# Kernel optimization log

Hardware: AMD Instinct MI355X
Metric: run time of the kernel (lower is better)

Reference implementation:

```python
import jax, jax.numpy as jnp
import numpy as np


def _pairwise_upper_dists(x):
    # x: [N, D] -> distances for all i<j pairs, shape [N*(N-1)/2]
    n = x.shape[0]
    sq = jnp.sum(x * x, axis=-1)                      # [N]
    d2 = sq[:, None] + sq[None, :] - 2.0 * (x @ x.T)  # [N, N]
    d2 = jnp.maximum(d2, 0.0)
    iu, ju = jnp.triu_indices(n, k=1)                 # matches combinations(range(n), 2)
    return jnp.sqrt(d2[iu, ju])


def setup_inputs() -> dict:
    key = jax.random.key(0)
    k1, k2 = jax.random.split(key)
    pred = jax.random.normal(k1, (1024, 8192), dtype=jnp.float32)
    target = jax.random.normal(k2, (1024, 8192), dtype=jnp.float32)
    return {"pred": pred, "target": target}


def reference(pred, target):
    # all_pairs_in_batch=True branch: Euclidean distance per pair, MSE between
    # the pred-distance vector and the target-distance vector.
    pred_d = _pairwise_upper_dists(pred)      # [P]
    target_d = _pairwise_upper_dists(target)  # [P]
    return jnp.mean((pred_d - target_d) ** 2)
```

## Files before the change

### kernel.cpp

```cpp
#include <hip/hip_runtime.h>
#include <hip/hip_bf16.h>
#include <hip/hip_fp16.h>

#define D 8192
#define NPAIR 523776.0

typedef short short8 __attribute__((ext_vector_type(8)));
typedef float f32x4 __attribute__((ext_vector_type(4)));
typedef _Float16 f16x8 __attribute__((ext_vector_type(8)));
typedef int int32x4 __attribute__((ext_vector_type(4)));

#define GLOAD_LDS(G, L) __builtin_amdgcn_global_load_lds( \
    (const __attribute__((address_space(1))) void*)(G),   \
    (__attribute__((address_space(3))) void*)(L), 16, 0, 0)

__device__ __forceinline__ short8 cvt8(const float4 a, const float4 b) {
    union { short8 s; __hip_bfloat162 h[4]; } u;
    u.h[0] = __float22bfloat162_rn(make_float2(a.x, a.y));
    u.h[1] = __float22bfloat162_rn(make_float2(a.z, a.w));
    u.h[2] = __float22bfloat162_rn(make_float2(b.x, b.y));
    u.h[3] = __float22bfloat162_rn(make_float2(b.z, b.w));
    return u.s;
}

__device__ __forceinline__ int q8(float x) {
    return __float2int_rn(fminf(fmaxf(x * 32.f, -127.f), 127.f));
}
__device__ __forceinline__ int pack4(float a, float b, float c, float d) {
    return (q8(a) & 255) | ((q8(b) & 255) << 8) | ((q8(c) & 255) << 16) | ((q8(d) & 255) << 24);
}

__device__ __forceinline__ void decode_bid(int bid, int& m, int& ti, int& tj, int& k0, int& nsteps) {
    int x = bid & 7, s = bid >> 3;
    m = x >> 2;
    int xr = x & 3;
    if (s < 16) {
        ti = tj = s & 7;
        int c = ((s >> 3) << 2) + xr;
        k0 = c * 1024; nsteps = 16;
    } else {
        int sp = s - 16;
        int c = (sp / 28) * 4 + xr;
        int tt = sp % 28;
        int a = 0;
        while (tt >= 7 - a) { tt -= 7 - a; ++a; }
        ti = a; tj = a + 1 + tt;
        k0 = c * 512; nsteps = 8;
    }
}
__device__ __forceinline__ int bid_off(int m, int tt, int c) {
    return (m * 4 + (c & 3)) + ((16 + (c >> 2) * 28 + tt) << 3);
}
__device__ __forceinline__ int bid_diag(int m, int dt, int c) {
    return (m * 4 + (c & 3)) + ((((c >> 2) << 3) + dt) << 3);
}

__global__ __launch_bounds__(256)
void convert_kernel(const float* __restrict__ pred, const float* __restrict__ tgt,
                    char* __restrict__ q) {
    const int idx = blockIdx.x * 256 + threadIdx.x;
    const int t = idx & 511;
    const int c = idx >> 9;
    const int m = c >> 10, p = (c >> 7) & 7, ks = c & 127;
    const int rl = t >> 2;
    const int s = (t & 3) ^ ((rl >> 1) & 3);
    const float* __restrict__ src = (m ? tgt : pred) + (size_t)(p * 128 + rl) * D + ks * 64 + s * 16;
    const float4 a = ((const float4*)src)[0];
    const float4 b = ((const float4*)src)[1];
    const float4 e = ((const float4*)src)[2];
    const float4 f = ((const float4*)src)[3];
    int32x4 o;
    o[0] = pack4(a.x, a.y, a.z, a.w);
    o[1] = pack4(b.x, b.y, b.z, b.w);
    o[2] = pack4(e.x, e.y, e.z, e.w);
    o[3] = pack4(f.x, f.y, f.z, f.w);
    *(int32x4*)(q + (size_t)c * 8192 + t * 16) = o;
}

#define STAGE(S, COFF) { \
    GLOAD_LDS(gAc + (size_t)(S) * 8192 + gsub, lsb + (COFF) + wid * 1024); \
    if (!same) GLOAD_LDS(gBc + (size_t)(S) * 8192 + gsub, lsb + (COFF) + 8192 + wid * 1024); \
}

#define GSTEP { \
    if (sp + 1 < nsteps) STAGE(sp + 1, cN); \
    { \
        const char* __restrict__ bA = lsb + cC; \
        const char* __restrict__ bB = lsb + cC + boff; \
        __builtin_amdgcn_s_setprio(1); \
        int32x4 b0 = *(const int32x4*)(bB + rbB + kby); \
        int32x4 b1 = *(const int32x4*)(bB + rbB + 1024 + kby); \
        _Pragma("unroll") \
        for (int mi = 0; mi < 4; ++mi) { \
            int32x4 af = *(const int32x4*)(bA + rbA + mi * 1024 + kby); \
            acc[mi][0] = __builtin_amdgcn_mfma_i32_16x16x64_i8(af, b0, acc[mi][0], 0, 0, 0); \
            acc[mi][1] = __builtin_amdgcn_mfma_i32_16x16x64_i8(af, b1, acc[mi][1], 0, 0, 0); \
        } \
        __builtin_amdgcn_s_setprio(0); \
    } \
    asm volatile("s_waitcnt vmcnt(0)" ::: "memory"); \
    __builtin_amdgcn_s_barrier(); \
    { int t_ = cC; cC = cN; cN = t_; } \
    ++sp; \
}

__global__ __launch_bounds__(512, 4)
void gram_kernel(const char* __restrict__ q, __half* __restrict__ part,
                 float* __restrict__ norms) {
    int m, ti, tj, k0, nsteps;
    decode_bid(blockIdx.x, m, ti, tj, k0, nsteps);
    const bool same = (ti == tj);

    __shared__ short ls[16384];
    char* lsb = (char*)ls;

    const int tid = threadIdx.x;
    const int lane = tid & 63;
    const int wid = tid >> 6;
    const int wr = wid >> 2, wc = wid & 3;

    const char* __restrict__ gAc = q + (size_t)(m * 1024 + ti * 128 + (k0 >> 6)) * 8192;
    const char* __restrict__ gBc = q + (size_t)(m * 1024 + tj * 128 + (k0 >> 6)) * 8192;
    const int gsub = wid * 1024 + lane * 16;

    const int boff = same ? 0 : 8192;
    const int rbA = (wr * 64 + (lane & 15)) * 64;
    const int rbB = (wc * 32 + (lane & 15)) * 64;
    const int kby = (((lane >> 4) ^ (((lane & 15) >> 1) & 3)) << 4);

    int32x4 zero = {0, 0, 0, 0};
    int32x4 acc[4][2];
#pragma unroll
    for (int mi = 0; mi < 4; ++mi) { acc[mi][0] = zero; acc[mi][1] = zero; }

    int cC = 0, cN = 16384;

    STAGE(0, cC)
    asm volatile("s_waitcnt vmcnt(0)" ::: "memory");
    __builtin_amdgcn_s_barrier();

    int sp = 0;
    while (sp < nsteps) { GSTEP }

    __half* __restrict__ dst = part + (size_t)blockIdx.x * 16384;
#pragma unroll
    for (int mi = 0; mi < 4; ++mi)
#pragma unroll
        for (int ni = 0; ni < 2; ++ni)
#pragma unroll
            for (int r = 0; r < 4; ++r) {
                int li = wr * 64 + mi * 16 + (lane >> 4) * 4 + r;
                int lj = wc * 32 + ni * 16 + (lane & 15);
                float g = (float)acc[mi][ni][r] * (1.f / 1024.f);
                dst[li * 128 + lj] = __float2half_rn(g);
                if (same && li == lj)
                    atomicAdd(&norms[m * 1024 + ti * 128 + li], g);
            }
}

__global__ __launch_bounds__(256)
void loss_store_kernel(const __half* __restrict__ part, const float* __restrict__ norms,
                       float* __restrict__ partial) {
    const int tid = threadIdx.x;
    const int sid = blockIdx.x * 256 + tid;
    const int i  = sid >> 7;
    const int j0 = (sid & 127) << 3;
    float local = 0.f;
    if (j0 + 7 > i) {
        const int ti = i >> 7, tj = j0 >> 7;
        const int el = ((i & 127) << 7) + (j0 & 127);
        float gp[8] = {0,0,0,0,0,0,0,0}, gt[8] = {0,0,0,0,0,0,0,0};
        if (ti == tj) {
#pragma unroll
            for (int c = 0; c < 8; ++c) {
                f16x8 vp = *(const f16x8*)(part + (size_t)bid_diag(0, ti, c) * 16384 + el);
                f16x8 vt = *(const f16x8*)(part + (size_t)bid_diag(1, ti, c) * 16384 + el);
#pragma unroll
                for (int e = 0; e < 8; ++e) { gp[e] += (float)vp[e]; gt[e] += (float)vt[e]; }
            }
        } else {
            int tt = 7 * ti - (ti * (ti - 1)) / 2 + (tj - ti - 1);
#pragma unroll
            for (int c = 0; c < 16; ++c) {
                f16x8 vp = *(const f16x8*)(part + (size_t)bid_off(0, tt, c) * 16384 + el);
                f16x8 vt = *(const f16x8*)(part + (size_t)bid_off(1, tt, c) * 16384 + el);
#pragma unroll
                for (int e = 0; e < 8; ++e) { gp[e] += (float)vp[e]; gt[e] += (float)vt[e]; }
            }
        }
        const float nip = norms[i], nit = norms[1024 + i];
        const float4 njp0 = *(const float4*)(norms + j0);
        const float4 njp1 = *(const float4*)(norms + j0 + 4);
        const float4 njt0 = *(const float4*)(norms + 1024 + j0);
        const float4 njt1 = *(const float4*)(norms + 1024 + j0 + 4);
        const float njp[8] = {njp0.x, njp0.y, njp0.z, njp0.w, njp1.x, njp1.y, njp1.z, njp1.w};
        const float njt[8] = {njt0.x, njt0.y, njt0.z, njt0.w, njt1.x, njt1.y, njt1.z, njt1.w};
#pragma unroll
        for (int e = 0; e < 8; ++e) {
            int j = j0 + e;
            if (j > i) {
                float dp = nip + njp[e] - 2.f * gp[e];
                float dt = nit + njt[e] - 2.f * gt[e];
                float c2 = sqrtf(fmaxf(dp, 0.f)) - sqrtf(fmaxf(dt, 0.f));
                local += c2 * c2;
            }
        }
    }
#pragma unroll
    for (int off = 32; off > 0; off >>= 1) local += __shfl_down(local, off);
    __shared__ float wsum[4];
    if ((tid & 63) == 0) wsum[tid >> 6] = local;
    __syncthreads();
    if (tid == 0) partial[blockIdx.x] = wsum[0] + wsum[1] + wsum[2] + wsum[3];
}

template<int NPART>
__global__ __launch_bounds__(256)
void finalize_kernel(const float* __restrict__ partial, float* __restrict__ out) {
    const int tid = threadIdx.x;
    double local = 0.0;
#pragma unroll
    for (int k = 0; k < NPART / 256; ++k) local += (double)partial[tid + k * 256];
#pragma unroll
    for (int off = 32; off > 0; off >>= 1) local += __shfl_down(local, off);
    __shared__ double wsum[4];
    if ((tid & 63) == 0) wsum[tid >> 6] = local;
    __syncthreads();
    if (tid == 0) out[0] = (float)((wsum[0] + wsum[1] + wsum[2] + wsum[3]) / NPAIR);
}

__device__ __forceinline__ void decode_bid_fb(int bid, int& m, int& ti, int& tj, int& k0, int& nsteps) {
    int x = bid & 7, s = bid >> 3;
    m = x >> 2;
    int xr = x & 3;
    if (s < 16) {
        ti = tj = s & 7;
        int c = ((s >> 3) << 2) + xr;
        k0 = c * 1024; nsteps = 32;
    } else {
        int sp = s - 16;
        int c = (sp / 28) * 4 + xr;
        int tt = sp % 28;
        int a = 0;
        while (tt >= 7 - a) { tt -= 7 - a; ++a; }
        ti = a; tj = a + 1 + tt;
        k0 = c * 512; nsteps = 16;
    }
}

__global__ __launch_bounds__(512)
void gram_fb(const float* __restrict__ pred, const float* __restrict__ tgt,
             float* __restrict__ g4) {
    int m, ti, tj, k0, nsteps;
    decode_bid_fb(blockIdx.x, m, ti, tj, k0, nsteps);
    const bool same = (ti == tj);
    const float* __restrict__ x = m ? tgt : pred;
    __shared__ short lsA[2][4096];
    __shared__ short lsB[2][4096];
    const int tid = threadIdx.x;
    const int lane = tid & 63;
    const int wid = tid >> 6;
    const int wr = wid >> 2, wc = wid & 3;
    const int srow = tid >> 2, sc8 = tid & 3;
    const float* __restrict__ gA = x + (size_t)(ti * 128 + srow) * D + k0 + sc8 * 8;
    const float* __restrict__ gB = x + (size_t)(tj * 128 + srow) * D + k0 + sc8 * 8;
    const int wby = srow * 64 + ((sc8 ^ ((srow >> 1) & 3)) << 4);
    const int rbA = (wr * 64 + (lane & 15)) * 64;
    const int rbB = (wc * 32 + (lane & 15)) * 64;
    const int kby = (((lane >> 4) ^ (((lane & 15) >> 1) & 3)) << 4);
    f32x4 zero = {0.f, 0.f, 0.f, 0.f};
    f32x4 acc[4][2];
#pragma unroll
    for (int mi = 0; mi < 4; ++mi) { acc[mi][0] = zero; acc[mi][1] = zero; }
    float4 ra0, ra1, rb0, rb1;
    { const float4* p = (const float4*)gA; ra0 = p[0]; ra1 = p[1];
      if (!same) { const float4* qq = (const float4*)gB; rb0 = qq[0]; rb1 = qq[1]; } }
    *(short8*)((char*)lsA[0] + wby) = cvt8(ra0, ra1);
    if (!same) *(short8*)((char*)lsB[0] + wby) = cvt8(rb0, rb1);
    { const float4* p = (const float4*)(gA + 32); ra0 = p[0]; ra1 = p[1];
      if (!same) { const float4* qq = (const float4*)(gB + 32); rb0 = qq[0]; rb1 = qq[1]; } }
    asm volatile("s_waitcnt lgkmcnt(0)" ::: "memory");
    __builtin_amdgcn_s_barrier();
    for (int step = 0; step < nsteps; ++step) {
        const int cur = step & 1;
        const short* __restrict__ bufA = lsA[cur];
        const short* __restrict__ bufB = same ? lsA[cur] : lsB[cur];
        short8 bf0 = *(const short8*)((const char*)bufB + (rbB + kby));
        short8 bf1 = *(const short8*)((const char*)bufB + (rbB + 1024 + kby));
#pragma unroll
        for (int mi = 0; mi < 4; ++mi) {
            short8 af = *(const short8*)((const char*)bufA + (rbA + mi * 1024 + kby));
            acc[mi][0] = __builtin_amdgcn_mfma_f32_16x16x32_bf16(af, bf0, acc[mi][0], 0, 0, 0);
            acc[mi][1] = __builtin_amdgcn_mfma_f32_16x16x32_bf16(af, bf1, acc[mi][1], 0, 0, 0);
        }
        if (step + 1 < nsteps) {
            const int nxt = cur ^ 1;
            *(short8*)((char*)lsA[nxt] + wby) = cvt8(ra0, ra1);
            if (!same) *(short8*)((char*)lsB[nxt] + wby) = cvt8(rb0, rb1);
            if (step + 2 < nsteps) {
                const float4* p = (const float4*)(gA + (step + 2) * 32);
                ra0 = p[0]; ra1 = p[1];
                if (!same) { const float4* qq = (const float4*)(gB + (step + 2) * 32); rb0 = qq[0]; rb1 = qq[1]; }
            }
        }
        asm volatile("s_waitcnt lgkmcnt(0)" ::: "memory");
        __builtin_amdgcn_s_barrier();
    }
#pragma unroll
    for (int mi = 0; mi < 4; ++mi)
#pragma unroll
        for (int ni = 0; ni < 2; ++ni)
#pragma unroll
            for (int r = 0; r < 4; ++r) {
                int gi = ti * 128 + wr * 64 + mi * 16 + (lane >> 4) * 4 + r;
                int gj = tj * 128 + wc * 32 + ni * 16 + (lane & 15);
                atomicAdd(&g4[(size_t)m * 1048576 + gi * 1024 + gj], acc[mi][ni][r]);
            }
}

__global__ __launch_bounds__(256)
void loss_atomic_kernel(const float* __restrict__ gram, float* __restrict__ partial) {
    const float* __restrict__ gP = gram;
    const float* __restrict__ gT = gram + 1024 * 1024;
    const int tid = threadIdx.x;
    const int base = blockIdx.x * 256 + tid;
    float local = 0.f;
#pragma unroll
    for (int s = 0; s < 4; ++s) {
        int lin = base + s * 262144;
        int i = lin >> 10, j = lin & 1023;
        if (j > i) {
            float dp = gP[i * 1024 + i] + gP[j * 1024 + j] - 2.f * gP[lin];
            float dt = gT[i * 1024 + i] + gT[j * 1024 + j] - 2.f * gT[lin];
            float c = sqrtf(fmaxf(dp, 0.f)) - sqrtf(fmaxf(dt, 0.f));
            local += c * c;
        }
    }
#pragma unroll
    for (int off = 32; off > 0; off >>= 1) local += __shfl_down(local, off);
    __shared__ float wsum[4];
    if ((tid & 63) == 0) wsum[tid >> 6] = local;
    __syncthreads();
    if (tid == 0) partial[blockIdx.x] = wsum[0] + wsum[1] + wsum[2] + wsum[3];
}

extern "C" void kernel_launch(void* const* d_in, const int* in_sizes, int n_in,
                              void* d_out, int out_size, void* d_ws, size_t ws_size,
                              hipStream_t stream) {
    const float* pred = (const float*)d_in[0];
    const float* tgt  = (const float*)d_in[1];
    const size_t q_bytes    = (size_t)2048 * 8192;
    const size_t part_bytes = (size_t)1024 * 16384 * 2;
    const size_t need = q_bytes + part_bytes + (2048 + 512) * sizeof(float);
    if (ws_size >= need) {
        char* qbuf     = (char*)d_ws;
        __half* part   = (__half*)((char*)d_ws + q_bytes);
        float* norms   = (float*)((char*)part + part_bytes);
        float* partial = norms + 2048;
        hipMemsetAsync(norms, 0, 2048 * sizeof(float), stream);
        convert_kernel<<<4096, 256, 0, stream>>>(pred, tgt, qbuf);
        gram_kernel<<<1024, 512, 0, stream>>>(qbuf, part, norms);
        loss_store_kernel<<<512, 256, 0, stream>>>(part, norms, partial);
        finalize_kernel<512><<<1, 256, 0, stream>>>(partial, (float*)d_out);
    } else {
        float* gram    = (float*)d_ws;
        float* partial = (float*)d_ws + (size_t)2 * 1024 * 1024;
        hipMemsetAsync(gram, 0, (size_t)2 * 1024 * 1024 * sizeof(float), stream);
        gram_fb<<<1024, 512, 0, stream>>>(pred, tgt, gram);
        loss_atomic_kernel<<<1024, 256, 0, stream>>>(gram, partial);
        finalize_kernel<1024><<<1, 256, 0, stream>>>(partial, (float*)d_out);
    }
}
```

Measured before the change: 48.50 us.

## Split gram K-range across twice as many blocks with single-shot LDS load

Doubles the number of gram blocks by halving each block's K slab (diagonal blocks cover 8 slabs, off-diagonal 4). Each block now loads its whole slab into a larger 64KB LDS buffer at once and computes without a double-buffered pipeline. This spreads work over more CUs and cuts the per-block serial steps. In exchange the loss kernel must reduce twice as many fp16 partial tiles, and the partial buffer doubles in size. The larger LDS footprint may also lower occupancy.

```diff
diff --git a/kernel.cpp b/kernel.cpp
--- a/kernel.cpp
+++ b/kernel.cpp
@@ -30,26 +30,26 @@
     return (q8(a) & 255) | ((q8(b) & 255) << 8) | ((q8(c) & 255) << 16) | ((q8(d) & 255) << 24);
 }
 
-__device__ __forceinline__ void decode_bid(int bid, int& m, int& ti, int& tj, int& k0, int& nsteps) {
+__device__ __forceinline__ void decode_bid(int bid, int& m, int& ti, int& tj, int& ks0, bool& diag) {
     int x = bid & 7, s = bid >> 3;
     m = x >> 2;
     int xr = x & 3;
-    if (s < 16) {
+    if (s < 32) {
         ti = tj = s & 7;
         int c = ((s >> 3) << 2) + xr;
-        k0 = c * 1024; nsteps = 16;
-    } else {
-        int sp = s - 16;
-        int c = (sp / 28) * 4 + xr;
+        ks0 = c * 8; diag = true;
+    } else {
+        int sp = s - 32;
+        int c = ((sp / 28) << 2) + xr;
         int tt = sp % 28;
         int a = 0;
         while (tt >= 7 - a) { tt -= 7 - a; ++a; }
         ti = a; tj = a + 1 + tt;
-        k0 = c * 512; nsteps = 8;
+        ks0 = c * 4; diag = false;
     }
 }
 __device__ __forceinline__ int bid_off(int m, int tt, int c) {
-    return (m * 4 + (c & 3)) + ((16 + (c >> 2) * 28 + tt) << 3);
+    return (m * 4 + (c & 3)) + ((32 + (c >> 2) * 28 + tt) << 3);
 }
 __device__ __forceinline__ int bid_diag(int m, int dt, int c) {
     return (m * 4 + (c & 3)) + ((((c >> 2) << 3) + dt) << 3);
@@ -77,41 +77,27 @@
     *(int32x4*)(q + (size_t)c * 8192 + t * 16) = o;
 }
 
-#define STAGE(S, COFF) { \
-    GLOAD_LDS(gAc + (size_t)(S) * 8192 + gsub, lsb + (COFF) + wid * 1024); \
-    if (!same) GLOAD_LDS(gBc + (size_t)(S) * 8192 + gsub, lsb + (COFF) + 8192 + wid * 1024); \
-}
-
-#define GSTEP { \
-    if (sp + 1 < nsteps) STAGE(sp + 1, cN); \
-    { \
-        const char* __restrict__ bA = lsb + cC; \
-        const char* __restrict__ bB = lsb + cC + boff; \
-        __builtin_amdgcn_s_setprio(1); \
-        int32x4 b0 = *(const int32x4*)(bB + rbB + kby); \
-        int32x4 b1 = *(const int32x4*)(bB + rbB + 1024 + kby); \
-        _Pragma("unroll") \
-        for (int mi = 0; mi < 4; ++mi) { \
-            int32x4 af = *(const int32x4*)(bA + rbA + mi * 1024 + kby); \
-            acc[mi][0] = __builtin_amdgcn_mfma_i32_16x16x64_i8(af, b0, acc[mi][0], 0, 0, 0); \
-            acc[mi][1] = __builtin_amdgcn_mfma_i32_16x16x64_i8(af, b1, acc[mi][1], 0, 0, 0); \
-        } \
-        __builtin_amdgcn_s_setprio(0); \
+#define COMPUTE_SLAB(SS, BOFF) { \
+    const char* __restrict__ bA = lsb + (SS) * 8192; \
+    const char* __restrict__ bB = lsb + (BOFF) + (SS) * 8192; \
+    int32x4 b0 = *(const int32x4*)(bB + rbB + kby); \
+    int32x4 b1 = *(const int32x4*)(bB + rbB + 1024 + kby); \
+    _Pragma("unroll") \
+    for (int mi = 0; mi < 4; ++mi) { \
+        int32x4 af = *(const int32x4*)(bA + rbA + mi * 1024 + kby); \
+        acc[mi][0] = __builtin_amdgcn_mfma_i32_16x16x64_i8(af, b0, acc[mi][0], 0, 0, 0); \
+        acc[mi][1] = __builtin_amdgcn_mfma_i32_16x16x64_i8(af, b1, acc[mi][1], 0, 0, 0); \
     } \
-    asm volatile("s_waitcnt vmcnt(0)" ::: "memory"); \
-    __builtin_amdgcn_s_barrier(); \
-    { int t_ = cC; cC = cN; cN = t_; } \
-    ++sp; \
 }
 
 __global__ __launch_bounds__(512, 4)
 void gram_kernel(const char* __restrict__ q, __half* __restrict__ part,
                  float* __restrict__ norms) {
-    int m, ti, tj, k0, nsteps;
-    decode_bid(blockIdx.x, m, ti, tj, k0, nsteps);
-    const bool same = (ti == tj);
-
-    __shared__ short ls[16384];
+    int m, ti, tj, ks0;
+    bool diag;
+    decode_bid(blockIdx.x, m, ti, tj, ks0, diag);
+
+    __shared__ short ls[32768];
     char* lsb = (char*)ls;
 
     const int tid = threadIdx.x;
@@ -119,11 +105,10 @@
     const int wid = tid >> 6;
     const int wr = wid >> 2, wc = wid & 3;
 
-    const char* __restrict__ gAc = q + (size_t)(m * 1024 + ti * 128 + (k0 >> 6)) * 8192;
-    const char* __restrict__ gBc = q + (size_t)(m * 1024 + tj * 128 + (k0 >> 6)) * 8192;
+    const char* __restrict__ gAc = q + (size_t)(m * 1024 + ti * 128 + ks0) * 8192;
+    const char* __restrict__ gBc = q + (size_t)(m * 1024 + tj * 128 + ks0) * 8192;
     const int gsub = wid * 1024 + lane * 16;
 
-    const int boff = same ? 0 : 8192;
     const int rbA = (wr * 64 + (lane & 15)) * 64;
     const int rbB = (wc * 32 + (lane & 15)) * 64;
     const int kby = (((lane >> 4) ^ (((lane & 15) >> 1) & 3)) << 4);
@@ -133,14 +118,29 @@
 #pragma unroll
     for (int mi = 0; mi < 4; ++mi) { acc[mi][0] = zero; acc[mi][1] = zero; }
 
-    int cC = 0, cN = 16384;
-
-    STAGE(0, cC)
+    if (diag) {
+#pragma unroll
+        for (int ss = 0; ss < 8; ++ss)
+            GLOAD_LDS(gAc + (size_t)ss * 8192 + gsub, lsb + ss * 8192 + wid * 1024);
+    } else {
+#pragma unroll
+        for (int ss = 0; ss < 4; ++ss) {
+            GLOAD_LDS(gAc + (size_t)ss * 8192 + gsub, lsb + ss * 8192 + wid * 1024);
+            GLOAD_LDS(gBc + (size_t)ss * 8192 + gsub, lsb + 32768 + ss * 8192 + wid * 1024);
+        }
+    }
     asm volatile("s_waitcnt vmcnt(0)" ::: "memory");
     __builtin_amdgcn_s_barrier();
 
-    int sp = 0;
-    while (sp < nsteps) { GSTEP }
+    __builtin_amdgcn_s_setprio(1);
+    if (diag) {
+#pragma unroll
+        for (int ss = 0; ss < 8; ++ss) COMPUTE_SLAB(ss, 0)
+    } else {
+#pragma unroll
+        for (int ss = 0; ss < 4; ++ss) COMPUTE_SLAB(ss, 32768)
+    }
+    __builtin_amdgcn_s_setprio(0);
 
     __half* __restrict__ dst = part + (size_t)blockIdx.x * 16384;
 #pragma unroll
@@ -153,7 +153,7 @@
                 int lj = wc * 32 + ni * 16 + (lane & 15);
                 float g = (float)acc[mi][ni][r] * (1.f / 1024.f);
                 dst[li * 128 + lj] = __float2half_rn(g);
-                if (same && li == lj)
+                if (diag && li == lj)
                     atomicAdd(&norms[m * 1024 + ti * 128 + li], g);
             }
 }
@@ -172,7 +172,7 @@
         float gp[8] = {0,0,0,0,0,0,0,0}, gt[8] = {0,0,0,0,0,0,0,0};
         if (ti == tj) {
 #pragma unroll
-            for (int c = 0; c < 8; ++c) {
+            for (int c = 0; c < 16; ++c) {
                 f16x8 vp = *(const f16x8*)(part + (size_t)bid_diag(0, ti, c) * 16384 + el);
                 f16x8 vt = *(const f16x8*)(part + (size_t)bid_diag(1, ti, c) * 16384 + el);
 #pragma unroll
@@ -181,7 +181,7 @@
         } else {
             int tt = 7 * ti - (ti * (ti - 1)) / 2 + (tj - ti - 1);
 #pragma unroll
-            for (int c = 0; c < 16; ++c) {
+            for (int c = 0; c < 32; ++c) {
                 f16x8 vp = *(const f16x8*)(part + (size_t)bid_off(0, tt, c) * 16384 + el);
                 f16x8 vt = *(const f16x8*)(part + (size_t)bid_off(1, tt, c) * 16384 + el);
 #pragma unroll
@@ -350,7 +350,7 @@
     const float* pred = (const float*)d_in[0];
     const float* tgt  = (const float*)d_in[1];
     const size_t q_bytes    = (size_t)2048 * 8192;
-    const size_t part_bytes = (size_t)1024 * 16384 * 2;
+    const size_t part_bytes = (size_t)2048 * 16384 * 2;
     const size_t need = q_bytes + part_bytes + (2048 + 512) * sizeof(float);
     if (ws_size >= need) {
         char* qbuf     = (char*)d_ws;
@@ -359,7 +359,7 @@
         float* partial = norms + 2048;
         hipMemsetAsync(norms, 0, 2048 * sizeof(float), stream);
         convert_kernel<<<4096, 256, 0, stream>>>(pred, tgt, qbuf);
-        gram_kernel<<<1024, 512, 0, stream>>>(qbuf, part, norms);
+        gram_kernel<<<2048, 512, 0, stream>>>(qbuf, part, norms);
         loss_store_kernel<<<512, 256, 0, stream>>>(part, norms, partial);
         finalize_kernel<512><<<1, 256, 0, stream>>>(partial, (float*)d_out);
     } else {
```

After: 60.89 us. +25.5%, slower.

## Stage gram tile epilogue through swizzled LDS for coalesced 16-byte stores

Applied to the files above, without the earlier changes.

The gram kernel epilogue used to write each fp16 result as a scattered 2-byte global store. It now writes the accumulators into LDS with an XOR swizzle, syncs, and copies the 128x128 tile out with 16-byte vector stores per thread. The diagonal norm atomics move into a separate pre-pass, and launch bounds now request 8 blocks per SM instead of 4. The extra barriers and LDS round trip add latency, and the tighter launch bound may force register spilling.

```diff
diff --git a/kernel.cpp b/kernel.cpp
--- a/kernel.cpp
+++ b/kernel.cpp
@@ -104,7 +104,7 @@
     ++sp; \
 }
 
-__global__ __launch_bounds__(512, 4)
+__global__ __launch_bounds__(512, 8)
 void gram_kernel(const char* __restrict__ q, __half* __restrict__ part,
                  float* __restrict__ norms) {
     int m, ti, tj, k0, nsteps;
@@ -142,7 +142,21 @@
     int sp = 0;
     while (sp < nsteps) { GSTEP }
 
-    __half* __restrict__ dst = part + (size_t)blockIdx.x * 16384;
+    if (same) {
+#pragma unroll
+        for (int mi = 0; mi < 4; ++mi)
+#pragma unroll
+            for (int ni = 0; ni < 2; ++ni)
+#pragma unroll
+                for (int r = 0; r < 4; ++r) {
+                    int li = wr * 64 + mi * 16 + (lane >> 4) * 4 + r;
+                    int lj = wc * 32 + ni * 16 + (lane & 15);
+                    if (li == lj)
+                        atomicAdd(&norms[m * 1024 + ti * 128 + li],
+                                  (float)acc[mi][ni][r] * (1.f / 1024.f));
+                }
+    }
+    __syncthreads();
 #pragma unroll
     for (int mi = 0; mi < 4; ++mi)
 #pragma unroll
@@ -151,11 +165,18 @@
             for (int r = 0; r < 4; ++r) {
                 int li = wr * 64 + mi * 16 + (lane >> 4) * 4 + r;
                 int lj = wc * 32 + ni * 16 + (lane & 15);
-                float g = (float)acc[mi][ni][r] * (1.f / 1024.f);
-                dst[li * 128 + lj] = __float2half_rn(g);
-                if (same && li == lj)
-                    atomicAdd(&norms[m * 1024 + ti * 128 + li], g);
-            }
+                int byte = li * 256 + ((lj * 2) ^ ((li & 7) << 4));
+                *(__half*)(lsb + byte) = __float2half_rn((float)acc[mi][ni][r] * (1.f / 1024.f));
+            }
+    __syncthreads();
+    char* __restrict__ dstb = (char*)(part + (size_t)blockIdx.x * 16384);
+#pragma unroll
+    for (int qq = 0; qq < 4; ++qq) {
+        int L = qq * 8192 + tid * 16;
+        int li = L >> 8;
+        f16x8 v = *(const f16x8*)(lsb + (L ^ ((li & 7) << 4)));
+        *(f16x8*)(dstb + L) = v;
+    }
 }
 
 __global__ __launch_bounds__(256)
```

After: 47.88 us, median of 2. Within noise of the previous version (-1.3%).
